# Kernel optimization log

Hardware: AMD Instinct MI355X
Metric: run time of the kernel (lower is better)

The kernel has to match this reference:

```python
import jax, jax.numpy as jnp
import numpy as np

C_S = 128
C_T = 128
C_OUT = 128


def _proj(x, W, b):
    # 1x1x1 Conv3d == per-voxel linear over channel dim. x: [B, Cin, T, H, W]
    return jnp.einsum('oc,bcthw->bothw', W, x) + b[None, :, None, None, None]


def setup_inputs() -> dict:
    key = jax.random.key(0)
    ks = jax.random.split(key, 12)
    B, T, H, W = 4, 4, 32, 32
    spatial_features = jax.random.normal(ks[0], (B, T, C_S, H, W), dtype=jnp.float32)
    temporal_features = jax.random.normal(ks[1], (B, C_T, T, H, W), dtype=jnp.float32)
    def w(k, o, i):
        return jax.random.normal(k, (o, i), dtype=jnp.float32) * (i ** -0.5)
    return {
        'spatial_features': spatial_features,
        'temporal_features': temporal_features,
        'Wq': w(ks[2], C_OUT, C_S), 'bq': jnp.zeros((C_OUT,), jnp.float32),
        'Wk': w(ks[3], C_OUT, C_T), 'bk': jnp.zeros((C_OUT,), jnp.float32),
        'Wv': w(ks[4], C_OUT, C_T), 'bv': jnp.zeros((C_OUT,), jnp.float32),
        'Wo': w(ks[5], C_OUT, C_OUT), 'bo': jnp.zeros((C_OUT,), jnp.float32),
    }


def reference(spatial_features, temporal_features, Wq, bq, Wk, bk, Wv, bv, Wo, bo):
    B, T, C_s, H, W = spatial_features.shape
    N = T * H * W
    scale = C_OUT ** -0.5
    # permute(0,2,1,3,4): [B, T, C_s, H, W] -> [B, C_s, T, H, W]
    x_s = jnp.transpose(spatial_features, (0, 2, 1, 3, 4))
    q = _proj(x_s, Wq, bq)                 # [B, C_out, T, H, W]
    k = _proj(temporal_features, Wk, bk)   # [B, C_out, T, H, W]
    v = _proj(temporal_features, Wv, bv)   # [B, C_out, T, H, W]
    Q = q.reshape(B, C_OUT, N).transpose(0, 2, 1)  # [B, N, C]
    K = k.reshape(B, C_OUT, N)                     # [B, C, N]
    V = v.reshape(B, C_OUT, N).transpose(0, 2, 1)  # [B, N, C]
    attn = jax.nn.softmax(jnp.einsum('bnc,bcm->bnm', Q, K) * scale, axis=2)  # [B, N, N]
    out = jnp.einsum('bnm,bmc->bnc', attn, V)      # [B, N, C]
    out = out.transpose(0, 2, 1).reshape(B, C_OUT, T, H, W)
    return _proj(out, Wo, bo)
```

## Files before the change

### kernel.cpp

```cpp
#include <hip/hip_runtime.h>
#include <cstddef>

#define NDIM 4096
#define SCALE 0.08838834764831843f
#define SOFT_BIAS 8.0f

typedef _Float16 h8 __attribute__((ext_vector_type(8)));
typedef _Float16 h4 __attribute__((ext_vector_type(4)));
typedef _Float16 h2 __attribute__((ext_vector_type(2)));
typedef float    f4 __attribute__((ext_vector_type(4)));

__device__ __forceinline__ h8 cvt_w_frag(const float* wp) {
    const float4 u0 = *(const float4*)wp;
    const float4 u1 = *(const float4*)(wp + 4);
    h8 f;
    f[0]=(_Float16)u0.x; f[1]=(_Float16)u0.y; f[2]=(_Float16)u0.z; f[3]=(_Float16)u0.w;
    f[4]=(_Float16)u1.x; f[5]=(_Float16)u1.y; f[6]=(_Float16)u1.z; f[7]=(_Float16)u1.w;
    return f;
}

__global__ __launch_bounds__(256) void prep_w_kernel(
    const float* __restrict__ Wq, const float* __restrict__ Wk,
    const float* __restrict__ Wv, const float* __restrict__ Wo,
    _Float16* __restrict__ Whf)
{
    const int gid = blockIdx.x * 256 + threadIdx.x;
    const int mat = gid >> 11, rem = gid & 2047;
    const int ot = rem >> 8, ks = (rem >> 6) & 3, l = rem & 63;
    const float* src = mat == 0 ? Wq : mat == 1 ? Wk : mat == 2 ? Wv : Wo;
    const h8 f = cvt_w_frag(src + (size_t)(16 * ot + (l & 15)) * 128 + 32 * ks + 8 * (l >> 4));
    *(h8*)(Whf + (size_t)gid * 8) = f;
}

__global__ __launch_bounds__(256, 3) void proj_qkv_kernel(
    const float* __restrict__ spatial, const float* __restrict__ temporal,
    const _Float16* __restrict__ Whf,
    const float* __restrict__ bq, const float* __restrict__ bk,
    const float* __restrict__ bv,
    _Float16* __restrict__ Qh, _Float16* __restrict__ Kh, _Float16* __restrict__ Vt)
{
    __shared__ __align__(16) _Float16 Xl[32 * 136];
    const int tid = threadIdx.x;
    const int n0  = blockIdx.x * 32;
    const int b   = blockIdx.y;
    const int p   = blockIdx.z;
    const float* __restrict__ bias = (p == 0) ? bq : (p == 1) ? bk : bv;

    {
        const float* src; size_t rs;
        if (p == 0) { const int t = n0 >> 10, hw0 = n0 & 1023;
            src = spatial + (((size_t)(b * 4 + t) * 128) << 10) + hw0; rs = 1024; }
        else { src = temporal + ((size_t)(b * 128) << 12) + n0; rs = 4096; }
        #pragma unroll
        for (int i = 0; i < 2; ++i) {
            const int ii = tid + 256 * i;
            const int c2 = ii >> 3, j = ii & 7;
            const float4 v0 = *(const float4*)(src + (size_t)(2 * c2) * rs + 4 * j);
            const float4 v1 = *(const float4*)(src + (size_t)(2 * c2 + 1) * rs + 4 * j);
            const float a0[4] = {v0.x, v0.y, v0.z, v0.w};
            const float a1[4] = {v1.x, v1.y, v1.z, v1.w};
            #pragma unroll
            for (int u = 0; u < 4; ++u) {
                h2 pk; pk[0] = (_Float16)a0[u]; pk[1] = (_Float16)a1[u];
                *(h2*)&Xl[(4 * j + u) * 136 + 2 * c2] = pk;
            }
        }
    }
    __syncthreads();

    const int w = tid >> 6, lane = tid & 63, n16 = tid & 15, q4 = (tid >> 4) & 3;

    h8 wf[2][4];
    #pragma unroll
    for (int otl = 0; otl < 2; ++otl)
        #pragma unroll
        for (int ks = 0; ks < 4; ++ks)
            wf[otl][ks] = *(const h8*)(Whf + ((size_t)(((p * 8 + 2 * w + otl) * 4 + ks)) << 9)
                                           + lane * 8);
    h8 xf[2][4];
    #pragma unroll
    for (int ns = 0; ns < 2; ++ns)
        #pragma unroll
        for (int ks = 0; ks < 4; ++ks)
            xf[ns][ks] = *(const h8*)&Xl[(16 * ns + n16) * 136 + 32 * ks + 8 * q4];

    if (p < 2) {
        f4 acc[2][2];
        #pragma unroll
        for (int i = 0; i < 2; ++i) { acc[i][0] = (f4)0.0f; acc[i][1] = (f4)0.0f; }
        #pragma unroll
        for (int otl = 0; otl < 2; ++otl)
            #pragma unroll
            for (int ns = 0; ns < 2; ++ns)
                #pragma unroll
                for (int ks = 0; ks < 4; ++ks)
                    acc[otl][ns] = __builtin_amdgcn_mfma_f32_16x16x32_f16(
                        wf[otl][ks], xf[ns][ks], acc[otl][ns], 0, 0, 0);
        _Float16* __restrict__ dst = (p == 0) ? Qh : Kh;
        #pragma unroll
        for (int otl = 0; otl < 2; ++otl) {
            const float4 bb = *(const float4*)&bias[16 * (2 * w + otl) + 4 * q4];
            #pragma unroll
            for (int ns = 0; ns < 2; ++ns) {
                h4 r;
                r[0]=(_Float16)(acc[otl][ns][0]+bb.x); r[1]=(_Float16)(acc[otl][ns][1]+bb.y);
                r[2]=(_Float16)(acc[otl][ns][2]+bb.z); r[3]=(_Float16)(acc[otl][ns][3]+bb.w);
                *(h4*)(dst + ((size_t)b * NDIM + n0 + 16 * ns + n16) * 128
                           + 16 * (2 * w + otl) + 4 * q4) = r;
            }
        }
    } else {
        f4 acc[2][2];
        #pragma unroll
        for (int i = 0; i < 2; ++i) { acc[i][0] = (f4)0.0f; acc[i][1] = (f4)0.0f; }
        #pragma unroll
        for (int ns = 0; ns < 2; ++ns)
            #pragma unroll
            for (int otl = 0; otl < 2; ++otl)
                #pragma unroll
                for (int ks = 0; ks < 4; ++ks)
                    acc[ns][otl] = __builtin_amdgcn_mfma_f32_16x16x32_f16(
                        xf[ns][ks], wf[otl][ks], acc[ns][otl], 0, 0, 0);
        #pragma unroll
        for (int ns = 0; ns < 2; ++ns)
            #pragma unroll
            for (int otl = 0; otl < 2; ++otl) {
                const float bb = bias[16 * (2 * w + otl) + n16];
                h4 r;
                r[0]=(_Float16)(acc[ns][otl][0]+bb); r[1]=(_Float16)(acc[ns][otl][1]+bb);
                r[2]=(_Float16)(acc[ns][otl][2]+bb); r[3]=(_Float16)(acc[ns][otl][3]+bb);
                *(h4*)(Vt + ((size_t)(b * 128 + 16 * (2 * w + otl) + n16) << 12)
                          + n0 + 16 * ns + 4 * q4) = r;
            }
    }
}

__global__ __launch_bounds__(256, 2) void attn_kernel(
    const _Float16* __restrict__ Qh, const _Float16* __restrict__ Kh,
    const _Float16* __restrict__ Vt, _Float16* __restrict__ Opart,
    float* __restrict__ lpart)
{
    __shared__ __align__(16) _Float16 sh[29184];

    const int tid  = threadIdx.x;
    const int w    = tid >> 6, lane = tid & 63;
    const int g    = w >> 1,  p    = w & 1;
    const int n16  = lane & 15, q4 = lane >> 4;
    const int b    = blockIdx.z, hf = blockIdx.y;
    const int n0   = blockIdx.x * 128;
    const int mb   = hf * 1024;

    h8 qf[4][4];
    {
        const _Float16* Qb = Qh + ((size_t)b * NDIM + n0 + 64 * g + n16) * 128;
        #pragma unroll
        for (int qs = 0; qs < 4; ++qs)
            #pragma unroll
            for (int ks = 0; ks < 4; ++ks)
                qf[qs][ks] = *(const h8*)(Qb + (size_t)(16 * qs) * 128 + 32 * ks + 8 * q4);
    }

    const int km  = tid >> 4, kc8 = (tid & 15) * 8;
    const int vc  = tid >> 2, vm8 = (tid & 3) * 8;
    const _Float16* kp = Kh + ((size_t)b * NDIM + mb + km) * 128 + kc8;
    const _Float16* vp = Vt + (((size_t)(b * 128 + vc)) << 12) + mb + vm8;

    int4 kreg0 = *(const int4*)kp;
    int4 kreg1 = *(const int4*)(kp + (size_t)16 * 128);
    int4 vreg0 = *(const int4*)vp;
    int4 vreg1 = *(const int4*)(vp + ((size_t)64 << 12));
    *(int4*)&sh[km * 136 + kc8]        = kreg0;
    *(int4*)&sh[(16 + km) * 136 + kc8] = kreg1;
    kp += 32 * 128;
    kreg0 = *(const int4*)kp;
    kreg1 = *(const int4*)(kp + (size_t)16 * 128);

    f4 oacc[4][4];
    #pragma unroll
    for (int i = 0; i < 4; ++i)
        #pragma unroll
        for (int j = 0; j < 4; ++j) oacc[i][j] = (f4)0.0f;
    float lsum[4] = {0.0f, 0.0f, 0.0f, 0.0f};

    for (int it = 0; it < 32; ++it) {
        __syncthreads();
        const int cur = it & 1, prv = cur ^ 1;
        _Float16* __restrict__ KB = sh + cur * 4352;
        _Float16* __restrict__ KO = sh + prv * 4352;
        _Float16* __restrict__ VB = sh + 8704  + cur * 5120;
        const _Float16* __restrict__ VP = sh + 8704 + prv * 5120;
        _Float16* __restrict__ Pg = sh + 18944 + cur * 5120 + g * 2560;
        const _Float16* __restrict__ Pp = sh + 18944 + prv * 5120 + g * 2560;

        if (it > 0) {
            h8 pf[4], vf[4];
            #pragma unroll
            for (int qs = 0; qs < 4; ++qs)
                pf[qs] = *(const h8*)&Pp[(16 * qs + n16) * 40 + 8 * q4];
            #pragma unroll
            for (int ct = 0; ct < 4; ++ct)
                vf[ct] = *(const h8*)&VP[(64 * p + 16 * ct + n16) * 40 + 8 * q4];
            #pragma unroll
            for (int qs = 0; qs < 4; ++qs)
                #pragma unroll
                for (int ct = 0; ct < 4; ++ct)
                    oacc[qs][ct] = __builtin_amdgcn_mfma_f32_16x16x32_f16(
                        pf[qs], vf[ct], oacc[qs][ct], 0, 0, 0);
        }

        {
            f4 sacc[4];
            #pragma unroll
            for (int qs = 0; qs < 4; ++qs) sacc[qs] = (f4)0.0f;
            #pragma unroll
            for (int ks = 0; ks < 4; ++ks) {
                const h8 kf = *(const h8*)&KB[(16 * p + n16) * 136 + 32 * ks + 8 * q4];
                #pragma unroll
                for (int qs = 0; qs < 4; ++qs)
                    sacc[qs] = __builtin_amdgcn_mfma_f32_16x16x32_f16(kf, qf[qs][ks], sacc[qs], 0, 0, 0);
            }
            #pragma unroll
            for (int qs = 0; qs < 4; ++qs) {
                h4 pk;
                #pragma unroll
                for (int r = 0; r < 4; ++r) {
                    const float e = __expf(fmaf(sacc[qs][r], SCALE, -SOFT_BIAS));
                    lsum[qs] += e;
                    pk[r] = (_Float16)e;
                }
                *(h4*)&Pg[(16 * qs + n16) * 40 + 16 * p + 4 * q4] = pk;
            }
        }

        *(int4*)&VB[vc * 40 + vm8]        = vreg0;
        *(int4*)&VB[(64 + vc) * 40 + vm8] = vreg1;
        if (it < 31) {
            *(int4*)&KO[km * 136 + kc8]        = kreg0;
            *(int4*)&KO[(16 + km) * 136 + kc8] = kreg1;
            vp += 32;
            vreg0 = *(const int4*)vp;
            vreg1 = *(const int4*)(vp + ((size_t)64 << 12));
        }
        if (it < 30) {
            kp += 32 * 128;
            kreg0 = *(const int4*)kp;
            kreg1 = *(const int4*)(kp + (size_t)16 * 128);
        }
    }

    __syncthreads();
    {
        const _Float16* __restrict__ Pp = sh + 18944 + 5120 + g * 2560;
        const _Float16* __restrict__ VP = sh + 8704  + 5120;
        h8 pf[4], vf[4];
        #pragma unroll
        for (int qs = 0; qs < 4; ++qs)
            pf[qs] = *(const h8*)&Pp[(16 * qs + n16) * 40 + 8 * q4];
        #pragma unroll
        for (int ct = 0; ct < 4; ++ct)
            vf[ct] = *(const h8*)&VP[(64 * p + 16 * ct + n16) * 40 + 8 * q4];
        #pragma unroll
        for (int qs = 0; qs < 4; ++qs)
            #pragma unroll
            for (int ct = 0; ct < 4; ++ct)
                oacc[qs][ct] = __builtin_amdgcn_mfma_f32_16x16x32_f16(
                    pf[qs], vf[ct], oacc[qs][ct], 0, 0, 0);
    }

    #pragma unroll
    for (int qs = 0; qs < 4; ++qs) {
        lsum[qs] += __shfl_xor(lsum[qs], 16, 64);
        lsum[qs] += __shfl_xor(lsum[qs], 32, 64);
    }
    if (q4 == 0) {
        float* lb = lpart + ((size_t)((hf * 2 + p) * 4 + b)) * NDIM + n0 + 64 * g;
        #pragma unroll
        for (int qs = 0; qs < 4; ++qs) lb[16 * qs + n16] = lsum[qs];
    }

    __syncthreads();
    #pragma unroll
    for (int qs = 0; qs < 4; ++qs)
        #pragma unroll
        for (int ct = 0; ct < 4; ++ct)
            #pragma unroll
            for (int r = 0; r < 4; ++r)
                sh[(64 * g + 16 * qs + 4 * q4 + r) * 136 + 64 * p + 16 * ct + n16] =
                    (_Float16)oacc[qs][ct][r];
    __syncthreads();
    const size_t ob = ((size_t)(hf * 4 + b) * NDIM + n0) * 128;
    #pragma unroll
    for (int i = 0; i < 8; ++i) {
        const int ii  = tid + 256 * i;
        const int row = ii >> 4, c8 = (ii & 15) * 8;
        *(int4*)(Opart + ob + (size_t)row * 128 + c8) = *(const int4*)&sh[row * 136 + c8];
    }
}

__global__ __launch_bounds__(256, 2) void proj_final_kernel(
    const _Float16* __restrict__ Opart, const float* __restrict__ lpart,
    const _Float16* __restrict__ Whf, const float* __restrict__ bo,
    float* __restrict__ out)
{
    __shared__ __align__(16) _Float16 Xl[32 * 136];
    __shared__ float lrow[32];
    __shared__ __align__(16) float Ofin[128 * 36];
    const int tid = threadIdx.x;
    const int n0  = blockIdx.x * 32;
    const int b   = blockIdx.y;

    if (tid < 32) {
        float l = 0.0f;
        #pragma unroll
        for (int h8i = 0; h8i < 8; ++h8i)
            l += lpart[((size_t)(h8i * 4 + b)) * NDIM + n0 + tid];
        lrow[tid] = 1.0f / l;
    }
    float vals[2][8];
    int rows[2], c8s[2];
    #pragma unroll
    for (int i = 0; i < 2; ++i) {
        const int ii = tid + 256 * i;
        rows[i] = ii >> 4; c8s[i] = (ii & 15) * 8;
        #pragma unroll
        for (int j = 0; j < 8; ++j) vals[i][j] = 0.0f;
        #pragma unroll
        for (int hf = 0; hf < 4; ++hf) {
            const h8 o = *(const h8*)(Opart + ((size_t)(hf * 4 + b) * NDIM + n0 + rows[i]) * 128
                                      + c8s[i]);
            #pragma unroll
            for (int j = 0; j < 8; ++j) vals[i][j] += (float)o[j];
        }
    }
    __syncthreads();
    #pragma unroll
    for (int i = 0; i < 2; ++i) {
        const float linv = lrow[rows[i]];
        h8 r;
        #pragma unroll
        for (int j = 0; j < 8; ++j) r[j] = (_Float16)(vals[i][j] * linv);
        *(h8*)&Xl[rows[i] * 136 + c8s[i]] = r;
    }
    __syncthreads();

    const int w = tid >> 6, lane = tid & 63, n16 = tid & 15, q4 = (tid >> 4) & 3;

    h8 wf[2][4];
    #pragma unroll
    for (int otl = 0; otl < 2; ++otl)
        #pragma unroll
        for (int ks = 0; ks < 4; ++ks)
            wf[otl][ks] = *(const h8*)(Whf + ((size_t)(((3 * 8 + 2 * w + otl) * 4 + ks)) << 9)
                                           + lane * 8);
    h8 xf[2][4];
    #pragma unroll
    for (int ns = 0; ns < 2; ++ns)
        #pragma unroll
        for (int ks = 0; ks < 4; ++ks)
            xf[ns][ks] = *(const h8*)&Xl[(16 * ns + n16) * 136 + 32 * ks + 8 * q4];

    f4 acc[2][2];
    #pragma unroll
    for (int i = 0; i < 2; ++i) { acc[i][0] = (f4)0.0f; acc[i][1] = (f4)0.0f; }
    #pragma unroll
    for (int otl = 0; otl < 2; ++otl)
        #pragma unroll
        for (int ns = 0; ns < 2; ++ns)
            #pragma unroll
            for (int ks = 0; ks < 4; ++ks)
                acc[otl][ns] = __builtin_amdgcn_mfma_f32_16x16x32_f16(
                    wf[otl][ks], xf[ns][ks], acc[otl][ns], 0, 0, 0);

    #pragma unroll
    for (int otl = 0; otl < 2; ++otl) {
        const float4 bb = *(const float4*)&bo[16 * (2 * w + otl) + 4 * q4];
        const float bias[4] = {bb.x, bb.y, bb.z, bb.w};
        #pragma unroll
        for (int ns = 0; ns < 2; ++ns)
            #pragma unroll
            for (int r = 0; r < 4; ++r)
                Ofin[(16 * (2 * w + otl) + 4 * q4 + r) * 36 + 16 * ns + n16] =
                    acc[otl][ns][r] + bias[r];
    }
    __syncthreads();
    #pragma unroll
    for (int i = 0; i < 4; ++i) {
        const int ii  = tid + 256 * i;
        const int row = ii >> 3, j = ii & 7;
        *(float4*)(out + (((size_t)(b * 128 + row)) << 12) + n0 + 4 * j) =
            *(const float4*)&Ofin[row * 36 + 4 * j];
    }
}

extern "C" void kernel_launch(void* const* d_in, const int* in_sizes, int n_in,
                              void* d_out, int out_size, void* d_ws, size_t ws_size,
                              hipStream_t stream)
{
    const float* spatial  = (const float*)d_in[0];
    const float* temporal = (const float*)d_in[1];
    const float* Wq = (const float*)d_in[2];
    const float* bq = (const float*)d_in[3];
    const float* Wk = (const float*)d_in[4];
    const float* bk = (const float*)d_in[5];
    const float* Wv = (const float*)d_in[6];
    const float* bv = (const float*)d_in[7];
    const float* Wo = (const float*)d_in[8];
    const float* bo = (const float*)d_in[9];

    char* ws = (char*)d_ws;
    _Float16* Qh    = (_Float16*)(ws);
    _Float16* Kh    = (_Float16*)(ws + (4u  << 20));
    _Float16* Vt    = (_Float16*)(ws + (8u  << 20));
    _Float16* Opart = (_Float16*)(ws + (12u << 20));
    float*    lpart = (float*)   (ws + (28u << 20));
    _Float16* Whf   = (_Float16*)(ws + (28u << 20) + (512u << 10));

    prep_w_kernel<<<32, 256, 0, stream>>>(Wq, Wk, Wv, Wo, Whf);
    proj_qkv_kernel<<<dim3(128, 4, 3), 256, 0, stream>>>(
        spatial, temporal, Whf, bq, bk, bv, Qh, Kh, Vt);
    attn_kernel<<<dim3(32, 4, 4), 256, 0, stream>>>(Qh, Kh, Vt, Opart, lpart);
    proj_final_kernel<<<dim3(128, 4), 256, 0, stream>>>(Opart, lpart, Whf, bo,
                                                        (float*)d_out);
}
```

Before: 136.1 us.

## Load K/V MFMA fragments directly from global, drop LDS staging, remap blocks

Result: slower. 161.8 us (+18.9%).

```diff
diff --git a/kernel.cpp b/kernel.cpp
--- a/kernel.cpp
+++ b/kernel.cpp
@@ -4,6 +4,8 @@
 #define NDIM 4096
 #define SCALE 0.08838834764831843f
 #define SOFT_BIAS 8.0f
+#define SCALE_L2E 0.12751741843533886f
+#define BIAS_L2E  11.541560327111707f
 
 typedef _Float16 h8 __attribute__((ext_vector_type(8)));
 typedef _Float16 h4 __attribute__((ext_vector_type(4)));
@@ -140,15 +142,19 @@
     const _Float16* __restrict__ Vt, _Float16* __restrict__ Opart,
     float* __restrict__ lpart)
 {
-    __shared__ __align__(16) _Float16 sh[29184];
+    __shared__ __align__(16) _Float16 sh[17408];
 
     const int tid  = threadIdx.x;
     const int w    = tid >> 6, lane = tid & 63;
     const int g    = w >> 1,  p    = w & 1;
     const int n16  = lane & 15, q4 = lane >> 4;
-    const int b    = blockIdx.z, hf = blockIdx.y;
-    const int n0   = blockIdx.x * 128;
-    const int mb   = hf * 1024;
+
+    const int id = blockIdx.x + 32 * blockIdx.y + 128 * blockIdx.z;
+    const int pi = (id & 7) + 8 * (id >> 8);
+    const int qt = (id >> 3) & 31;
+    const int hf = pi & 3, b = pi >> 2;
+    const int n0 = qt * 128;
+    const int mb = hf * 1024;
 
     h8 qf[4][4];
     {
@@ -160,20 +166,13 @@
                 qf[qs][ks] = *(const h8*)(Qb + (size_t)(16 * qs) * 128 + 32 * ks + 8 * q4);
     }
 
-    const int km  = tid >> 4, kc8 = (tid & 15) * 8;
-    const int vc  = tid >> 2, vm8 = (tid & 3) * 8;
-    const _Float16* kp = Kh + ((size_t)b * NDIM + mb + km) * 128 + kc8;
-    const _Float16* vp = Vt + (((size_t)(b * 128 + vc)) << 12) + mb + vm8;
-
-    int4 kreg0 = *(const int4*)kp;
-    int4 kreg1 = *(const int4*)(kp + (size_t)16 * 128);
-    int4 vreg0 = *(const int4*)vp;
-    int4 vreg1 = *(const int4*)(vp + ((size_t)64 << 12));
-    *(int4*)&sh[km * 136 + kc8]        = kreg0;
-    *(int4*)&sh[(16 + km) * 136 + kc8] = kreg1;
-    kp += 32 * 128;
-    kreg0 = *(const int4*)kp;
-    kreg1 = *(const int4*)(kp + (size_t)16 * 128);
+    const _Float16* kb = Kh + ((size_t)b * NDIM + mb + 16 * p + n16) * 128 + 8 * q4;
+    const _Float16* vb = Vt + (((size_t)(b * 128 + 64 * p + n16)) << 12) + mb + 8 * q4;
+
+    h8 kfr[4], vfr[4];
+    #pragma unroll
+    for (int ks = 0; ks < 4; ++ks)
+        kfr[ks] = *(const h8*)(kb + 32 * ks);
 
     f4 oacc[4][4];
     #pragma unroll
@@ -184,87 +183,74 @@
 
     for (int it = 0; it < 32; ++it) {
         __syncthreads();
-        const int cur = it & 1, prv = cur ^ 1;
-        _Float16* __restrict__ KB = sh + cur * 4352;
-        _Float16* __restrict__ KO = sh + prv * 4352;
-        _Float16* __restrict__ VB = sh + 8704  + cur * 5120;
-        const _Float16* __restrict__ VP = sh + 8704 + prv * 5120;
-        _Float16* __restrict__ Pg = sh + 18944 + cur * 5120 + g * 2560;
-        const _Float16* __restrict__ Pp = sh + 18944 + prv * 5120 + g * 2560;
+        const int cur = it & 1;
+        _Float16* __restrict__ Pg = sh + cur * 5120 + g * 2560;
+        const _Float16* __restrict__ Pp = sh + (cur ^ 1) * 5120 + g * 2560;
 
         if (it > 0) {
-            h8 pf[4], vf[4];
+            h8 pf[4];
             #pragma unroll
             for (int qs = 0; qs < 4; ++qs)
                 pf[qs] = *(const h8*)&Pp[(16 * qs + n16) * 40 + 8 * q4];
-            #pragma unroll
-            for (int ct = 0; ct < 4; ++ct)
-                vf[ct] = *(const h8*)&VP[(64 * p + 16 * ct + n16) * 40 + 8 * q4];
             #pragma unroll
             for (int qs = 0; qs < 4; ++qs)
                 #pragma unroll
                 for (int ct = 0; ct < 4; ++ct)
                     oacc[qs][ct] = __builtin_amdgcn_mfma_f32_16x16x32_f16(
-                        pf[qs], vf[ct], oacc[qs][ct], 0, 0, 0);
+                        pf[qs], vfr[ct], oacc[qs][ct], 0, 0, 0);
         }
 
         {
-            f4 sacc[4];
-            #pragma unroll
-            for (int qs = 0; qs < 4; ++qs) sacc[qs] = (f4)0.0f;
-            #pragma unroll
-            for (int ks = 0; ks < 4; ++ks) {
-                const h8 kf = *(const h8*)&KB[(16 * p + n16) * 136 + 32 * ks + 8 * q4];
-                #pragma unroll
-                for (int qs = 0; qs < 4; ++qs)
-                    sacc[qs] = __builtin_amdgcn_mfma_f32_16x16x32_f16(kf, qf[qs][ks], sacc[qs], 0, 0, 0);
+            const _Float16* vt = vb + 32 * it;
+            #pragma unroll
+            for (int ct = 0; ct < 4; ++ct)
+                vfr[ct] = *(const h8*)(vt + ((size_t)ct << 16));
+        }
+
+        f4 sacc[4];
+        #pragma unroll
+        for (int qs = 0; qs < 4; ++qs) sacc[qs] = (f4)0.0f;
+        #pragma unroll
+        for (int ks = 0; ks < 4; ++ks) {
+            const h8 kf = kfr[ks];
+            #pragma unroll
+            for (int qs = 0; qs < 4; ++qs)
+                sacc[qs] = __builtin_amdgcn_mfma_f32_16x16x32_f16(kf, qf[qs][ks], sacc[qs], 0, 0, 0);
+        }
+
+        if (it < 31) {
+            kb += 32 * 128;
+            #pragma unroll
+            for (int ks = 0; ks < 4; ++ks)
+                kfr[ks] = *(const h8*)(kb + 32 * ks);
+        }
+
+        #pragma unroll
+        for (int qs = 0; qs < 4; ++qs) {
+            h4 pk;
+            #pragma unroll
+            for (int r = 0; r < 4; ++r) {
+                const float e = __builtin_amdgcn_exp2f(fmaf(sacc[qs][r], SCALE_L2E, -BIAS_L2E));
+                lsum[qs] += e;
+                pk[r] = (_Float16)e;
             }
-            #pragma unroll
-            for (int qs = 0; qs < 4; ++qs) {
-                h4 pk;
-                #pragma unroll
-                for (int r = 0; r < 4; ++r) {
-                    const float e = __expf(fmaf(sacc[qs][r], SCALE, -SOFT_BIAS));
-                    lsum[qs] += e;
-                    pk[r] = (_Float16)e;
-                }
-                *(h4*)&Pg[(16 * qs + n16) * 40 + 16 * p + 4 * q4] = pk;
-            }
-        }
-
-        *(int4*)&VB[vc * 40 + vm8]        = vreg0;
-        *(int4*)&VB[(64 + vc) * 40 + vm8] = vreg1;
-        if (it < 31) {
-            *(int4*)&KO[km * 136 + kc8]        = kreg0;
-            *(int4*)&KO[(16 + km) * 136 + kc8] = kreg1;
-            vp += 32;
-            vreg0 = *(const int4*)vp;
-            vreg1 = *(const int4*)(vp + ((size_t)64 << 12));
-        }
-        if (it < 30) {
-            kp += 32 * 128;
-            kreg0 = *(const int4*)kp;
-            kreg1 = *(const int4*)(kp + (size_t)16 * 128);
+            *(h4*)&Pg[(16 * qs + n16) * 40 + 16 * p + 4 * q4] = pk;
         }
     }
 
     __syncthreads();
     {
-        const _Float16* __restrict__ Pp = sh + 18944 + 5120 + g * 2560;
-        const _Float16* __restrict__ VP = sh + 8704  + 5120;
-        h8 pf[4], vf[4];
+        const _Float16* __restrict__ Pp = sh + 5120 + g * 2560;
+        h8 pf[4];
         #pragma unroll
         for (int qs = 0; qs < 4; ++qs)
             pf[qs] = *(const h8*)&Pp[(16 * qs + n16) * 40 + 8 * q4];
         #pragma unroll
-        for (int ct = 0; ct < 4; ++ct)
-            vf[ct] = *(const h8*)&VP[(64 * p + 16 * ct + n16) * 40 + 8 * q4];
-        #pragma unroll
         for (int qs = 0; qs < 4; ++qs)
             #pragma unroll
             for (int ct = 0; ct < 4; ++ct)
                 oacc[qs][ct] = __builtin_amdgcn_mfma_f32_16x16x32_f16(
-                    pf[qs], vf[ct], oacc[qs][ct], 0, 0, 0);
+                    pf[qs], vfr[ct], oacc[qs][ct], 0, 0, 0);
     }
 
     #pragma unroll
```
